# Kernel tuning notes

Hardware: AMD Instinct MI355X
Metric: run time of the kernel (lower is better)

## Reference

```python
import jax, jax.numpy as jnp
import numpy as np

B, N, C_IN = 4, 48, 32
HID = [32, 32]          # hidden_channel_list
NB = [32, 32]           # neighborhood_channels
C_OUT = 16
N_BASIS = 6             # equivariant 2->2 basis ops used by SnConv2


def _masked(t, mask):
    # zero out entries for padded nodes; mask: B,n,n,n bool, t: B,n,n,n,C
    return jnp.where(mask[..., None], t, jnp.zeros((), t.dtype))


def snconv2(t, W, b):
    """Sn-equivariant 2nd-order conv on dims (1,2); dim 3 rides along.
    t: B,i,j,m,C.  W: [6, C_in, C_out], one mixing matrix per basis op."""
    n = t.shape[1]
    tT = jnp.swapaxes(t, 1, 2)                       # transpose op
    diag = jnp.einsum('biimc->bimc', t)              # diagonal, B,i,m,C
    rows = t.sum(axis=2) / n                         # row sums,  B,i,m,C
    cols = t.sum(axis=1) / n                         # col sums,  B,j,m,C
    tot = t.sum(axis=(1, 2)) / (n * n)               # total sum, B,m,C
    # contract small features BEFORE broadcasting back to 2nd order
    out = (jnp.einsum('bijmc,cd->bijmd', t, W[0])
           + jnp.einsum('bijmc,cd->bijmd', tT, W[1])
           + jnp.einsum('bimc,cd->bimd', diag, W[2])[:, :, None]
           + jnp.einsum('bimc,cd->bimd', rows, W[3])[:, :, None]
           + jnp.einsum('bjmc,cd->bjmd', cols, W[4])[:, None]
           + jnp.einsum('bmc,cd->bmd', tot, W[5])[:, None, None]
           + b)
    return out


def localconv2(t, Wv, bv, Ww, bw, Wo, bo):
    """LocalConv2, product_type='elementwise': per-channel message passing
    along the node dims: z[b,i,j] = sum_k v[b,i,k] * w[b,k,j] / n."""
    n = t.shape[1]
    v = jnp.einsum('bijmc,cd->bijmd', t, Wv) + bv
    w = jnp.einsum('bijmc,cd->bijmd', t, Ww) + bw
    z = jnp.einsum('bikmc,bkjmc->bijmc', v, w) / n
    return jnp.einsum('bijmc,cd->bijmd', z, Wo) + bo


def setup_inputs() -> dict:
    key = jax.random.key(0)
    ks = jax.random.split(key, 24)
    x = jax.random.normal(ks[0], (B, N, C_IN), dtype=jnp.float32)
    # graphs of unequal size: per-graph node counts in [N//2, N]
    sizes = jax.random.randint(ks[1], (B,), N // 2, N + 1)
    node_valid = jnp.arange(N)[None, :] < sizes[:, None]            # B,n
    mask = (node_valid[:, :, None, None]
            & node_valid[:, None, :, None]
            & node_valid[:, None, None, :])                          # B,n,n,n
    s = 0.05
    inp = {'x': x, 'mask': mask}
    cin = C_IN
    for li, (nch, cout) in enumerate(zip(NB, HID)):
        inp[f'basic_W{li}'] = s * jax.random.normal(ks[2 + 8 * li], (N_BASIS, cin, cin), dtype=jnp.float32)
        inp[f'basic_b{li}'] = jnp.zeros((cin,), jnp.float32)
        inp[f'lv_W{li}'] = s * jax.random.normal(ks[3 + 8 * li], (cin, nch), dtype=jnp.float32)
        inp[f'lv_b{li}'] = jnp.zeros((nch,), jnp.float32)
        inp[f'lw_W{li}'] = s * jax.random.normal(ks[4 + 8 * li], (cin, nch), dtype=jnp.float32)
        inp[f'lw_b{li}'] = jnp.zeros((nch,), jnp.float32)
        inp[f'lo_W{li}'] = s * jax.random.normal(ks[5 + 8 * li], (nch, cout), dtype=jnp.float32)
        inp[f'lo_b{li}'] = jnp.zeros((cout,), jnp.float32)
        cin = cout
    inp['final_W'] = s * jax.random.normal(ks[20], (N_BASIS, cin, C_OUT), dtype=jnp.float32)
    inp['final_b'] = jnp.zeros((C_OUT,), jnp.float32)
    return inp


def reference(x, mask,
              basic_W0, basic_b0, lv_W0, lv_b0, lw_W0, lw_b0, lo_W0, lo_b0,
              basic_W1, basic_b1, lv_W1, lv_b1, lw_W1, lw_b1, lo_W1, lo_b1,
              final_W, final_b):
    # order-3 outer product T[b,i,j,k,c] = x[b,i,c]*x[b,j,c]*x[b,k,c]
    t = (x[:, :, None, None, :] * x[:, None, :, None, :]) * x[:, None, None, :, :]
    t = _masked(t, mask)
    layers = [(basic_W0, basic_b0, lv_W0, lv_b0, lw_W0, lw_b0, lo_W0, lo_b0),
              (basic_W1, basic_b1, lv_W1, lv_b1, lw_W1, lw_b1, lo_W1, lo_b1)]
    for bw_, bb_, vw, vb, ww, wb, ow, ob in layers:
        t = _masked(snconv2(t, bw_, bb_), mask)
        t = localconv2(t, vw, vb, ww, wb, ow, ob)
        t = jax.nn.relu(t)
        t = _masked(t, mask)
    out = _masked(snconv2(t, final_W, final_b), mask)
    return out
```

## Files before the change

kernel.cpp:

```cpp
#include <hip/hip_runtime.h>
#include <cstdint>


namespace {

constexpr int nB = 4, nN = 48, nC = 32;
constexpr int SJ_ = nN * nC;
constexpr int SI_ = nN * SJ_;
constexpr long SB_ = (long)nN * SI_;
constexpr int CP_ = 294912;
constexpr int TP_ = 6144;

__device__ __forceinline__ void decodePos(int p, int& b, int& i, int& j, int& m) {
    m = p % nN; int r = p / nN;
    j = r % nN; r /= nN;
    i = r % nN; b = r / nN;
}

__global__ __launch_bounds__(256) void k_prep(const float* __restrict__ x,
                                              const void* __restrict__ maskp,
                                              float* __restrict__ vm,
                                              float* __restrict__ S)
{
    __shared__ float vmL[nB * nN];
    const int tid = threadIdx.x;
    const unsigned int w0 = *(const unsigned int*)maskp;
    const bool is_byte = (w0 == 0x01010101u);
    if (tid < nB * nN) {
        int b = tid / nN, i = tid % nN;
        long idx = ((long)(b * nN + i) * nN + i) * nN + i;
        int bit;
        if (is_byte) bit = (((const unsigned char*)maskp)[idx] != 0);
        else         bit = (((const int*)maskp)[idx] != 0);
        float f = bit ? 1.f : 0.f;
        vm[tid] = f; vmL[tid] = f;
    }
    __syncthreads();
    if (tid < nB * nC) {
        int b = tid >> 5, c = tid & 31;
        float s = 0.f;
        for (int j = 0; j < nN; ++j) s += x[(b * nN + j) * nC + c] * vmL[b * nN + j];
        S[tid] = s;
    }
}

__global__ __launch_bounds__(256) void k_mix0(
    const float* __restrict__ x, const float* __restrict__ S,
    const float* __restrict__ Wb, const float* __restrict__ bias,
    float* __restrict__ drp, float* __restrict__ ccp, float* __restrict__ tbp)
{
    __shared__ float W2s[1024], W3s[1024], W4s[1024], W5s[1024], bs[32];
    const int tid = threadIdx.x;
    for (int q = tid; q < 1024; q += 256) {
        W2s[q] = Wb[2048 + q]; W3s[q] = Wb[3072 + q];
        W4s[q] = Wb[4096 + q]; W5s[q] = Wb[5120 + q];
    }
    if (tid < 32) bs[tid] = bias[tid];
    __syncthreads();
    const int id = blockIdx.x * 256 + tid;
    const int m = id % nN; int r = id / nN; const int i = r % nN; const int b = r / nN;
    float odr[32], occ[32];
    #pragma unroll
    for (int d = 0; d < 32; ++d) { odr[d] = 0.f; occ[d] = 0.f; }
    for (int c2 = 0; c2 < 32; ++c2) {
        float xi = x[(b * nN + i) * nC + c2];
        float xm = x[(b * nN + m) * nC + c2];
        float sc = S[b * nC + c2];
        float A = xi * xi * xm;
        float R = xi * xm * sc * (1.f / nN);
        #pragma unroll
        for (int d = 0; d < 32; ++d) {
            odr[d] = fmaf(A, W2s[c2 * 32 + d], fmaf(R, W3s[c2 * 32 + d], odr[d]));
            occ[d] = fmaf(R, W4s[c2 * 32 + d], occ[d]);
        }
    }
    #pragma unroll
    for (int d = 0; d < 32; d += 4) {
        *(float4*)(drp + (size_t)id * 32 + d) = make_float4(odr[d], odr[d+1], odr[d+2], odr[d+3]);
        *(float4*)(ccp + (size_t)id * 32 + d) = make_float4(occ[d], occ[d+1], occ[d+2], occ[d+3]);
    }
    if (i == 0) {
        float ot[32];
        #pragma unroll
        for (int d = 0; d < 32; ++d) ot[d] = bs[d];
        for (int c2 = 0; c2 < 32; ++c2) {
            float xm = x[(b * nN + m) * nC + c2];
            float sc = S[b * nC + c2];
            float Tc = xm * sc * sc * (1.f / (nN * nN));
            #pragma unroll
            for (int d = 0; d < 32; ++d) ot[d] = fmaf(Tc, W5s[c2 * 32 + d], ot[d]);
        }
        for (int d = 0; d < 32; d += 4)
            *(float4*)(tbp + (size_t)(b * nN + m) * 32 + d) = make_float4(ot[d], ot[d+1], ot[d+2], ot[d+3]);
    }
}

template <int DOUT>
__global__ __launch_bounds__(256) void k_mix(
    const float* __restrict__ dgp, const float* __restrict__ rwp,
    const float* __restrict__ clp4, const float* __restrict__ ttp4,
    const float* __restrict__ Wb, const float* __restrict__ bias,
    float* __restrict__ drp, float* __restrict__ ccp, float* __restrict__ tbp)
{
    __shared__ float W2s[32 * DOUT], W3s[32 * DOUT], W4s[32 * DOUT], W5s[32 * DOUT], bs[DOUT];
    const int tid = threadIdx.x;
    for (int q = tid; q < 32 * DOUT; q += 256) {
        W2s[q] = Wb[2 * 32 * DOUT + q]; W3s[q] = Wb[3 * 32 * DOUT + q];
        W4s[q] = Wb[4 * 32 * DOUT + q]; W5s[q] = Wb[5 * 32 * DOUT + q];
    }
    if (tid < DOUT) bs[tid] = bias[tid];
    __syncthreads();
    const int id = blockIdx.x * 256 + tid;
    const int m = id % nN; int r = id / nN; const int i = r % nN; const int b = r / nN;
    float odr[DOUT], occ[DOUT];
    #pragma unroll
    for (int d = 0; d < DOUT; ++d) { odr[d] = 0.f; occ[d] = 0.f; }
    for (int c2 = 0; c2 < 32; ++c2) {
        size_t q = (size_t)id * 32 + c2;
        float dg = dgp[q];
        float rw = rwp[q];
        float cl = clp4[q] + clp4[q + CP_] + clp4[q + 2 * CP_] + clp4[q + 3 * CP_];
        #pragma unroll
        for (int d = 0; d < DOUT; ++d) {
            odr[d] = fmaf(dg, W2s[c2 * DOUT + d], fmaf(rw, W3s[c2 * DOUT + d], odr[d]));
            occ[d] = fmaf(cl, W4s[c2 * DOUT + d], occ[d]);
        }
    }
    #pragma unroll
    for (int d = 0; d < DOUT; d += 4) {
        *(float4*)(drp + (size_t)id * DOUT + d) = make_float4(odr[d], odr[d+1], odr[d+2], odr[d+3]);
        *(float4*)(ccp + (size_t)id * DOUT + d) = make_float4(occ[d], occ[d+1], occ[d+2], occ[d+3]);
    }
    if (i == 0) {
        float ot[DOUT];
        #pragma unroll
        for (int d = 0; d < DOUT; ++d) ot[d] = bs[d];
        for (int c2 = 0; c2 < 32; ++c2) {
            size_t q = (size_t)(b * nN + m) * 32 + c2;
            float tv = ttp4[q] + ttp4[q + TP_] + ttp4[q + 2 * TP_] + ttp4[q + 3 * TP_];
            #pragma unroll
            for (int d = 0; d < DOUT; ++d) ot[d] = fmaf(tv, W5s[c2 * DOUT + d], ot[d]);
        }
        for (int d = 0; d < DOUT; d += 4)
            *(float4*)(tbp + (size_t)(b * nN + m) * DOUT + d) = make_float4(ot[d], ot[d+1], ot[d+2], ot[d+3]);
    }
}

__global__ __launch_bounds__(256) void k_red4(
    const float* __restrict__ t,
    float* __restrict__ rows_, float* __restrict__ cols4,
    float* __restrict__ diag_, float* __restrict__ tot4)
{
    const int blk = blockIdx.x;
    const int iq = blk & 3; const int bm = blk >> 2;
    const int b = bm / nN, m = bm % nN;
    const int jg = threadIdx.x >> 5;
    const int c = threadIdx.x & 31;
    __shared__ float part[8][32];
    const size_t base = (size_t)b * SB_ + (size_t)m * nC;
    float colacc[6] = {0, 0, 0, 0, 0, 0};
    float totacc = 0.f;
    for (int ii = 0; ii < 12; ++ii) {
        const int i = iq * 12 + ii;
        float vals[6];
        #pragma unroll
        for (int jl = 0; jl < 6; ++jl) {
            int j = jg * 6 + jl;
            vals[jl] = t[base + (size_t)i * SI_ + (size_t)j * SJ_ + c];
        }
        float rp = 0.f;
        #pragma unroll
        for (int jl = 0; jl < 6; ++jl) { colacc[jl] += vals[jl]; rp += vals[jl]; }
        {
            int jd = i - jg * 6;
            if (jd >= 0 && jd < 6) diag_[((size_t)(b * nN + i) * nN + m) * nC + c] = vals[jd];
        }
        part[jg][c] = rp;
        __syncthreads();
        if (jg == 0) {
            float rv = 0.f;
            #pragma unroll
            for (int g = 0; g < 8; ++g) rv += part[g][c];
            rows_[((size_t)(b * nN + i) * nN + m) * nC + c] = rv * (1.f / nN);
            totacc += rv;
        }
        __syncthreads();
    }
    #pragma unroll
    for (int jl = 0; jl < 6; ++jl) {
        int j = jg * 6 + jl;
        cols4[(size_t)iq * CP_ + ((size_t)(b * nN + j) * nN + m) * nC + c] = colacc[jl] * (1.f / nN);
    }
    if (jg == 0)
        tot4[(size_t)iq * TP_ + (size_t)(b * nN + m) * nC + c] = totacc * (1.f / (nN * nN));
}

template <int MODE>
__global__ __launch_bounds__(256) void k_vw(
    const float* __restrict__ src, const float* __restrict__ vm,
    const float* __restrict__ drp, const float* __restrict__ ccp, const float* __restrict__ tbp,
    const float* __restrict__ W0, const float* __restrict__ W1,
    const float* __restrict__ Wv, const float* __restrict__ bv,
    const float* __restrict__ Ww, const float* __restrict__ bw,
    float* __restrict__ vout, float* __restrict__ wout)
{
    __shared__ float sA[128 * 34];
    __shared__ float sB[(MODE == 0) ? 64 : 128 * 34];
    __shared__ float sS[128 * 34];
    const int tid = threadIdx.x;
    const long base = (long)blockIdx.x * 128;

    if (MODE == 0) {
        for (int rep = 0; rep < 4; ++rep) {
            int q = rep * 256 + tid; int pl = q >> 3, cq = q & 7;
            int p = (int)base + pl;
            int b, i, j, m; decodePos(p, b, i, j, m);
            float4 xi = *(const float4*)(src + (size_t)(b * nN + i) * nC + cq * 4);
            float4 xj = *(const float4*)(src + (size_t)(b * nN + j) * nC + cq * 4);
            float4 xm = *(const float4*)(src + (size_t)(b * nN + m) * nC + cq * 4);
            int o = pl * 34 + cq * 4;
            sA[o + 0] = xi.x * xj.x * xm.x;
            sA[o + 1] = xi.y * xj.y * xm.y;
            sA[o + 2] = xi.z * xj.z * xm.z;
            sA[o + 3] = xi.w * xj.w * xm.w;
        }
    } else {
        for (int rep = 0; rep < 4; ++rep) {
            int q = rep * 256 + tid; int pl = q >> 3, cq = q & 7;
            long p = base + pl;
            float4 a = *(const float4*)(src + p * nC + cq * 4);
            int o = pl * 34 + cq * 4;
            sA[o + 0] = a.x; sA[o + 1] = a.y; sA[o + 2] = a.z; sA[o + 3] = a.w;
            int b, i, j, m; decodePos((int)p, b, i, j, m);
            long pT = ((long)(b * nN + j) * nN + i) * nN + m;
            float4 t4 = *(const float4*)(src + pT * nC + cq * 4);
            sB[o + 0] = t4.x; sB[o + 1] = t4.y; sB[o + 2] = t4.z; sB[o + 3] = t4.w;
        }
    }
    __syncthreads();

    const int pt = tid >> 3, dq = tid & 7;
    const int p0 = pt * 4, d0 = dq * 4;
    float wc[32][4];
    float acc[4][4];

    auto zeroAcc = [&]() {
        #pragma unroll
        for (int a2 = 0; a2 < 4; ++a2)
            #pragma unroll
            for (int l = 0; l < 4; ++l) acc[a2][l] = 0.f;
    };
    auto loadW = [&](const float* Wp) {
        #pragma unroll
        for (int c2 = 0; c2 < 32; ++c2) {
            float4 q4 = *(const float4*)(Wp + c2 * nC + d0);
            wc[c2][0] = q4.x; wc[c2][1] = q4.y; wc[c2][2] = q4.z; wc[c2][3] = q4.w;
        }
    };
    auto addW = [&](const float* Wp) {
        #pragma unroll
        for (int c2 = 0; c2 < 32; ++c2) {
            float4 q4 = *(const float4*)(Wp + c2 * nC + d0);
            wc[c2][0] += q4.x; wc[c2][1] += q4.y; wc[c2][2] += q4.z; wc[c2][3] += q4.w;
        }
    };
    auto sweep = [&](const float* sp) {
        #pragma unroll
        for (int c2 = 0; c2 < 32; ++c2) {
            float t0 = sp[(p0 + 0) * 34 + c2];
            float t1 = sp[(p0 + 1) * 34 + c2];
            float t2 = sp[(p0 + 2) * 34 + c2];
            float t3 = sp[(p0 + 3) * 34 + c2];
            #pragma unroll
            for (int l = 0; l < 4; ++l) {
                acc[0][l] = fmaf(t0, wc[c2][l], acc[0][l]);
                acc[1][l] = fmaf(t1, wc[c2][l], acc[1][l]);
                acc[2][l] = fmaf(t2, wc[c2][l], acc[2][l]);
                acc[3][l] = fmaf(t3, wc[c2][l], acc[3][l]);
            }
        }
    };

    zeroAcc();
    if (MODE == 0) { loadW(W0); addW(W1); sweep(sA); }
    else           { loadW(W0); sweep(sA); loadW(W1); sweep(sB); }

    #pragma unroll
    for (int l = 0; l < 4; ++l) {
        int p = (int)base + p0 + l;
        int b, i, j, m; decodePos(p, b, i, j, m);
        float4 d4 = *(const float4*)(drp + (size_t)((b * nN + i) * nN + m) * nC + d0);
        float4 c4 = *(const float4*)(ccp + (size_t)((b * nN + j) * nN + m) * nC + d0);
        float4 t4 = *(const float4*)(tbp + (size_t)(b * nN + m) * nC + d0);
        float mk = vm[b * nN + i] * vm[b * nN + j] * vm[b * nN + m];
        int o = (p0 + l) * 34 + d0;
        sS[o + 0] = (acc[l][0] + d4.x + c4.x + t4.x) * mk;
        sS[o + 1] = (acc[l][1] + d4.y + c4.y + t4.y) * mk;
        sS[o + 2] = (acc[l][2] + d4.z + c4.z + t4.z) * mk;
        sS[o + 3] = (acc[l][3] + d4.w + c4.w + t4.w) * mk;
    }
    __syncthreads();

    zeroAcc(); loadW(Wv); sweep(sS);
    {
        float4 b4 = *(const float4*)(bv + d0);
        #pragma unroll
        for (int l = 0; l < 4; ++l) {
            float4 o4 = make_float4(acc[l][0] + b4.x, acc[l][1] + b4.y,
                                    acc[l][2] + b4.z, acc[l][3] + b4.w);
            *(float4*)(vout + (size_t)(base + p0 + l) * nC + d0) = o4;
        }
    }
    zeroAcc(); loadW(Ww); sweep(sS);
    {
        float4 b4 = *(const float4*)(bw + d0);
        #pragma unroll
        for (int l = 0; l < 4; ++l) {
            float4 o4 = make_float4(acc[l][0] + b4.x, acc[l][1] + b4.y,
                                    acc[l][2] + b4.z, acc[l][3] + b4.w);
            *(float4*)(wout + (size_t)(base + p0 + l) * nC + d0) = o4;
        }
    }
}

__global__ __launch_bounds__(256, 3) void k_z(
    const float* __restrict__ v, const float* __restrict__ w,
    const float* __restrict__ Wo, const float* __restrict__ bo,
    const float* __restrict__ vm, float* __restrict__ tout)
{
    __shared__ float lds[12912];
    float* Vt = lds;
    float* Wt = lds + 6456;
    const int tid = threadIdx.x;
    const int blk = blockIdx.x;
    const int tl = blk & 3; const int bm = blk >> 2;
    const int it = tl >> 1, jt = tl & 1;
    const int b = bm / nN, m = bm % nN;
    const int c = tid & 31;
    const int g = tid >> 5;
    const int i3 = g >> 1, j2 = g & 1;
    const int il0 = i3 * 6, jl0 = j2 * 12;
    const size_t posbase = (size_t)b * SB_ + (size_t)m * nC;

    float acc[6][12];
    #pragma unroll
    for (int l = 0; l < 6; ++l)
        #pragma unroll
        for (int u = 0; u < 12; ++u) acc[l][u] = 0.f;

    for (int kc = 0; kc < 6; ++kc) {
        if (kc) __syncthreads();
        #pragma unroll
        for (int rr = 0; rr < 6; ++rr) {
            int q = rr * 256 + tid; int pos = q >> 3, cq = q & 7;
            int ii = pos >> 3, kk = pos & 7;
            float4 a = *(const float4*)(v + posbase + (size_t)(it * 24 + ii) * SI_
                                          + (size_t)(kc * 8 + kk) * SJ_ + cq * 4);
            float* dst = Vt + kk * 807 + (cq * 4) * 25 + ii;
            dst[0] = a.x; dst[25] = a.y; dst[50] = a.z; dst[75] = a.w;
        }
        #pragma unroll
        for (int rr = 0; rr < 6; ++rr) {
            int q = rr * 256 + tid; int pos = q >> 3, cq = q & 7;
            int kk = pos / 24, jj = pos - kk * 24;
            float4 a = *(const float4*)(w + posbase + (size_t)(kc * 8 + kk) * SI_
                                          + (size_t)(jt * 24 + jj) * SJ_ + cq * 4);
            float* dst = Wt + kk * 807 + (cq * 4) * 25 + jj;
            dst[0] = a.x; dst[25] = a.y; dst[50] = a.z; dst[75] = a.w;
        }
        __syncthreads();
        #pragma unroll
        for (int kk = 0; kk < 8; ++kk) {
            float vf[6], wf[12];
            #pragma unroll
            for (int l = 0; l < 6; ++l) vf[l] = Vt[kk * 807 + c * 25 + il0 + l];
            #pragma unroll
            for (int u = 0; u < 12; ++u) wf[u] = Wt[kk * 807 + c * 25 + jl0 + u];
            #pragma unroll
            for (int l = 0; l < 6; ++l)
                #pragma unroll
                for (int u = 0; u < 12; ++u)
                    acc[l][u] = fmaf(vf[l], wf[u], acc[l][u]);
        }
    }
    __syncthreads();

    #pragma unroll
    for (int e = 0; e < 4; ++e)
        lds[9504 + e * 256 + tid] = Wo[e * 256 + tid] * (1.f / nN);

    const int ptE = tid >> 3, dqE = tid & 7, d0 = dqE * 4;
    const float4 b4 = *(const float4*)(bo + d0);
    const float vmm = vm[b * nN + m];

    for (int h = 0; h < 2; ++h) {
        if ((i3 >> 1) == h) {
            int r0 = il0 - 12 * h;
            #pragma unroll
            for (int l = 0; l < 6; ++l)
                #pragma unroll
                for (int u = 0; u < 12; ++u)
                    lds[((r0 + l) * 24 + jl0 + u) * 33 + c] = acc[l][u];
        }
        __syncthreads();

        float oac[9][4];
        #pragma unroll
        for (int u = 0; u < 9; ++u)
            #pragma unroll
            for (int d = 0; d < 4; ++d) oac[u][d] = 0.f;
        #pragma unroll
        for (int c2 = 0; c2 < 32; ++c2) {
            float4 wo4 = *(const float4*)(lds + 9504 + c2 * 32 + d0);
            float zv[9];
            #pragma unroll
            for (int u = 0; u < 9; ++u) zv[u] = lds[(ptE * 9 + u) * 33 + c2];
            #pragma unroll
            for (int u = 0; u < 9; ++u) {
                oac[u][0] = fmaf(zv[u], wo4.x, oac[u][0]);
                oac[u][1] = fmaf(zv[u], wo4.y, oac[u][1]);
                oac[u][2] = fmaf(zv[u], wo4.z, oac[u][2]);
                oac[u][3] = fmaf(zv[u], wo4.w, oac[u][3]);
            }
        }
        #pragma unroll
        for (int u = 0; u < 9; ++u) {
            int p = ptE * 9 + u;
            int rl = p / 24, jl = p - rl * 24;
            int gi = it * 24 + 12 * h + rl, gj = jt * 24 + jl;
            float mk = vm[b * nN + gi] * vm[b * nN + gj] * vmm;
            float4 o4;
            o4.x = fmaxf(oac[u][0] + b4.x, 0.f) * mk;
            o4.y = fmaxf(oac[u][1] + b4.y, 0.f) * mk;
            o4.z = fmaxf(oac[u][2] + b4.z, 0.f) * mk;
            o4.w = fmaxf(oac[u][3] + b4.w, 0.f) * mk;
            *(float4*)(tout + posbase + (size_t)gi * SI_ + (size_t)gj * SJ_ + d0) = o4;
        }
        if (h == 0) __syncthreads();
    }
}

__global__ __launch_bounds__(256) void k_final(
    const float* __restrict__ t, const float* __restrict__ vm,
    const float* __restrict__ drp, const float* __restrict__ ccp, const float* __restrict__ tbp,
    const float* __restrict__ W0, const float* __restrict__ W1,
    float* __restrict__ out)
{
    __shared__ float sA[128 * 34], sB[128 * 34];
    const int tid = threadIdx.x;
    const long base = (long)blockIdx.x * 128;
    for (int rep = 0; rep < 4; ++rep) {
        int q = rep * 256 + tid; int pl = q >> 3, cq = q & 7;
        long p = base + pl;
        float4 a = *(const float4*)(t + p * nC + cq * 4);
        int o = pl * 34 + cq * 4;
        sA[o + 0] = a.x; sA[o + 1] = a.y; sA[o + 2] = a.z; sA[o + 3] = a.w;
        int b, i, j, m; decodePos((int)p, b, i, j, m);
        long pT = ((long)(b * nN + j) * nN + i) * nN + m;
        float4 t4 = *(const float4*)(t + pT * nC + cq * 4);
        sB[o + 0] = t4.x; sB[o + 1] = t4.y; sB[o + 2] = t4.z; sB[o + 3] = t4.w;
    }
    __syncthreads();
    const int pt = tid >> 3, dq = tid & 7;
    const int p0 = pt * 4, d0 = dq * 2;
    float wc[32][2], acc[4][2];
    #pragma unroll
    for (int l = 0; l < 4; ++l) { acc[l][0] = 0.f; acc[l][1] = 0.f; }

    #pragma unroll
    for (int c2 = 0; c2 < 32; ++c2) {
        float2 q2 = *(const float2*)(W0 + c2 * 16 + d0);
        wc[c2][0] = q2.x; wc[c2][1] = q2.y;
    }
    #pragma unroll
    for (int c2 = 0; c2 < 32; ++c2) {
        float t0 = sA[(p0 + 0) * 34 + c2], t1 = sA[(p0 + 1) * 34 + c2];
        float t2 = sA[(p0 + 2) * 34 + c2], t3 = sA[(p0 + 3) * 34 + c2];
        acc[0][0] = fmaf(t0, wc[c2][0], acc[0][0]); acc[0][1] = fmaf(t0, wc[c2][1], acc[0][1]);
        acc[1][0] = fmaf(t1, wc[c2][0], acc[1][0]); acc[1][1] = fmaf(t1, wc[c2][1], acc[1][1]);
        acc[2][0] = fmaf(t2, wc[c2][0], acc[2][0]); acc[2][1] = fmaf(t2, wc[c2][1], acc[2][1]);
        acc[3][0] = fmaf(t3, wc[c2][0], acc[3][0]); acc[3][1] = fmaf(t3, wc[c2][1], acc[3][1]);
    }
    #pragma unroll
    for (int c2 = 0; c2 < 32; ++c2) {
        float2 q2 = *(const float2*)(W1 + c2 * 16 + d0);
        wc[c2][0] = q2.x; wc[c2][1] = q2.y;
    }
    #pragma unroll
    for (int c2 = 0; c2 < 32; ++c2) {
        float t0 = sB[(p0 + 0) * 34 + c2], t1 = sB[(p0 + 1) * 34 + c2];
        float t2 = sB[(p0 + 2) * 34 + c2], t3 = sB[(p0 + 3) * 34 + c2];
        acc[0][0] = fmaf(t0, wc[c2][0], acc[0][0]); acc[0][1] = fmaf(t0, wc[c2][1], acc[0][1]);
        acc[1][0] = fmaf(t1, wc[c2][0], acc[1][0]); acc[1][1] = fmaf(t1, wc[c2][1], acc[1][1]);
        acc[2][0] = fmaf(t2, wc[c2][0], acc[2][0]); acc[2][1] = fmaf(t2, wc[c2][1], acc[2][1]);
        acc[3][0] = fmaf(t3, wc[c2][0], acc[3][0]); acc[3][1] = fmaf(t3, wc[c2][1], acc[3][1]);
    }
    #pragma unroll
    for (int l = 0; l < 4; ++l) {
        int p = (int)base + p0 + l;
        int b, i, j, m; decodePos(p, b, i, j, m);
        float2 d2 = *(const float2*)(drp + (size_t)((b * nN + i) * nN + m) * 16 + d0);
        float2 cc2 = *(const float2*)(ccp + (size_t)((b * nN + j) * nN + m) * 16 + d0);
        float2 tb2 = *(const float2*)(tbp + (size_t)(b * nN + m) * 16 + d0);
        float mk = vm[b * nN + i] * vm[b * nN + j] * vm[b * nN + m];
        float2 o2;
        o2.x = (acc[l][0] + d2.x + cc2.x + tb2.x) * mk;
        o2.y = (acc[l][1] + d2.y + cc2.y + tb2.y) * mk;
        *(float2*)(out + (size_t)p * 16 + d0) = o2;
    }
}

}

extern "C" void kernel_launch(void* const* d_in, const int* in_sizes, int n_in,
                              void* d_out, int out_size, void* d_ws, size_t ws_size,
                              hipStream_t stream)
{
    (void)in_sizes; (void)n_in; (void)out_size; (void)ws_size;
    const float* x    = (const float*)d_in[0];
    const void*  mask = d_in[1];
    const float* bW0  = (const float*)d_in[2];
    const float* bb0  = (const float*)d_in[3];
    const float* lvW0 = (const float*)d_in[4];
    const float* lvb0 = (const float*)d_in[5];
    const float* lwW0 = (const float*)d_in[6];
    const float* lwb0 = (const float*)d_in[7];
    const float* loW0 = (const float*)d_in[8];
    const float* lob0 = (const float*)d_in[9];
    const float* bW1  = (const float*)d_in[10];
    const float* bb1  = (const float*)d_in[11];
    const float* lvW1 = (const float*)d_in[12];
    const float* lvb1 = (const float*)d_in[13];
    const float* lwW1 = (const float*)d_in[14];
    const float* lwb1 = (const float*)d_in[15];
    const float* loW1 = (const float*)d_in[16];
    const float* lob1 = (const float*)d_in[17];
    const float* fW   = (const float*)d_in[18];
    const float* fb   = (const float*)d_in[19];

    float* ws  = (float*)d_ws;
    float* t     = ws;
    float* v     = ws + 14155776L;
    float* w     = ws + 28311552L;
    float* rows  = ws + 42467328L;
    float* cols4 = rows + 294912;
    float* diag  = cols4 + 4 * 294912;
    float* tot4  = diag + 294912;
    float* dr    = tot4 + 4 * 6144;
    float* cc    = dr + 294912;
    float* tb    = cc + 294912;
    float* S     = tb + 6144;
    float* vm    = S + 128;
    float* out   = (float*)d_out;

    k_prep<<<1, 256, 0, stream>>>(x, mask, vm, S);
    k_mix0<<<36, 256, 0, stream>>>(x, S, bW0, bb0, dr, cc, tb);
    k_vw<0><<<3456, 256, 0, stream>>>(x, vm, dr, cc, tb, bW0, bW0 + 1024,
                                      lvW0, lvb0, lwW0, lwb0, v, w);
    k_z<<<768, 256, 0, stream>>>(v, w, loW0, lob0, vm, t);
    k_red4<<<768, 256, 0, stream>>>(t, rows, cols4, diag, tot4);
    k_mix<32><<<36, 256, 0, stream>>>(diag, rows, cols4, tot4, bW1, bb1, dr, cc, tb);

    k_vw<1><<<3456, 256, 0, stream>>>(t, vm, dr, cc, tb, bW1, bW1 + 1024,
                                      lvW1, lvb1, lwW1, lwb1, v, w);
    k_z<<<768, 256, 0, stream>>>(v, w, loW1, lob1, vm, t);
    k_red4<<<768, 256, 0, stream>>>(t, rows, cols4, diag, tot4);
    k_mix<16><<<36, 256, 0, stream>>>(diag, rows, cols4, tot4, fW, fb, dr, cc, tb);
    k_final<<<3456, 256, 0, stream>>>(t, vm, dr, cc, tb, fW, fW + 512, out);
}
```

Before: 537.7 us.

## Fuse row/col/diag/total reductions into k_z epilogue, drop k_red4

```diff
diff --git a/kernel.cpp b/kernel.cpp
--- a/kernel.cpp
+++ b/kernel.cpp
@@ -8,6 +8,7 @@
 constexpr int SJ_ = nN * nC;
 constexpr int SI_ = nN * SJ_;
 constexpr long SB_ = (long)nN * SI_;
+constexpr int RP_ = 294912;
 constexpr int CP_ = 294912;
 constexpr int TP_ = 6144;
 
@@ -97,8 +98,8 @@
 
 template <int DOUT>
 __global__ __launch_bounds__(256) void k_mix(
-    const float* __restrict__ dgp, const float* __restrict__ rwp,
-    const float* __restrict__ clp4, const float* __restrict__ ttp4,
+    const float* __restrict__ dgp, const float* __restrict__ rw2,
+    const float* __restrict__ cl2, const float* __restrict__ tt4,
     const float* __restrict__ Wb, const float* __restrict__ bias,
     float* __restrict__ drp, float* __restrict__ ccp, float* __restrict__ tbp)
 {
@@ -118,8 +119,8 @@
     for (int c2 = 0; c2 < 32; ++c2) {
         size_t q = (size_t)id * 32 + c2;
         float dg = dgp[q];
-        float rw = rwp[q];
-        float cl = clp4[q] + clp4[q + CP_] + clp4[q + 2 * CP_] + clp4[q + 3 * CP_];
+        float rw = (rw2[q] + rw2[q + RP_]) * (1.f / nN);
+        float cl = (cl2[q] + cl2[q + CP_]) * (1.f / nN);
         #pragma unroll
         for (int d = 0; d < DOUT; ++d) {
             odr[d] = fmaf(dg, W2s[c2 * DOUT + d], fmaf(rw, W3s[c2 * DOUT + d], odr[d]));
@@ -137,62 +138,14 @@
         for (int d = 0; d < DOUT; ++d) ot[d] = bs[d];
         for (int c2 = 0; c2 < 32; ++c2) {
             size_t q = (size_t)(b * nN + m) * 32 + c2;
-            float tv = ttp4[q] + ttp4[q + TP_] + ttp4[q + 2 * TP_] + ttp4[q + 3 * TP_];
+            float tv = (tt4[q] + tt4[q + TP_] + tt4[q + 2 * TP_] + tt4[q + 3 * TP_])
+                       * (1.f / (nN * nN));
             #pragma unroll
             for (int d = 0; d < DOUT; ++d) ot[d] = fmaf(tv, W5s[c2 * DOUT + d], ot[d]);
         }
         for (int d = 0; d < DOUT; d += 4)
             *(float4*)(tbp + (size_t)(b * nN + m) * DOUT + d) = make_float4(ot[d], ot[d+1], ot[d+2], ot[d+3]);
     }
-}
-
-__global__ __launch_bounds__(256) void k_red4(
-    const float* __restrict__ t,
-    float* __restrict__ rows_, float* __restrict__ cols4,
-    float* __restrict__ diag_, float* __restrict__ tot4)
-{
-    const int blk = blockIdx.x;
-    const int iq = blk & 3; const int bm = blk >> 2;
-    const int b = bm / nN, m = bm % nN;
-    const int jg = threadIdx.x >> 5;
-    const int c = threadIdx.x & 31;
-    __shared__ float part[8][32];
-    const size_t base = (size_t)b * SB_ + (size_t)m * nC;
-    float colacc[6] = {0, 0, 0, 0, 0, 0};
-    float totacc = 0.f;
-    for (int ii = 0; ii < 12; ++ii) {
-        const int i = iq * 12 + ii;
-        float vals[6];
-        #pragma unroll
-        for (int jl = 0; jl < 6; ++jl) {
-            int j = jg * 6 + jl;
-            vals[jl] = t[base + (size_t)i * SI_ + (size_t)j * SJ_ + c];
-        }
-        float rp = 0.f;
-        #pragma unroll
-        for (int jl = 0; jl < 6; ++jl) { colacc[jl] += vals[jl]; rp += vals[jl]; }
-        {
-            int jd = i - jg * 6;
-            if (jd >= 0 && jd < 6) diag_[((size_t)(b * nN + i) * nN + m) * nC + c] = vals[jd];
-        }
-        part[jg][c] = rp;
-        __syncthreads();
-        if (jg == 0) {
-            float rv = 0.f;
-            #pragma unroll
-            for (int g = 0; g < 8; ++g) rv += part[g][c];
-            rows_[((size_t)(b * nN + i) * nN + m) * nC + c] = rv * (1.f / nN);
-            totacc += rv;
-        }
-        __syncthreads();
-    }
-    #pragma unroll
-    for (int jl = 0; jl < 6; ++jl) {
-        int j = jg * 6 + jl;
-        cols4[(size_t)iq * CP_ + ((size_t)(b * nN + j) * nN + m) * nC + c] = colacc[jl] * (1.f / nN);
-    }
-    if (jg == 0)
-        tot4[(size_t)iq * TP_ + (size_t)(b * nN + m) * nC + c] = totacc * (1.f / (nN * nN));
 }
 
 template <int MODE>
@@ -266,17 +219,22 @@
     };
     auto sweep = [&](const float* sp) {
         #pragma unroll
-        for (int c2 = 0; c2 < 32; ++c2) {
-            float t0 = sp[(p0 + 0) * 34 + c2];
-            float t1 = sp[(p0 + 1) * 34 + c2];
-            float t2 = sp[(p0 + 2) * 34 + c2];
-            float t3 = sp[(p0 + 3) * 34 + c2];
-            #pragma unroll
-            for (int l = 0; l < 4; ++l) {
-                acc[0][l] = fmaf(t0, wc[c2][l], acc[0][l]);
-                acc[1][l] = fmaf(t1, wc[c2][l], acc[1][l]);
-                acc[2][l] = fmaf(t2, wc[c2][l], acc[2][l]);
-                acc[3][l] = fmaf(t3, wc[c2][l], acc[3][l]);
+        for (int cp = 0; cp < 16; ++cp) {
+            float2 t0 = *(const float2*)(sp + (p0 + 0) * 34 + cp * 2);
+            float2 t1 = *(const float2*)(sp + (p0 + 1) * 34 + cp * 2);
+            float2 t2 = *(const float2*)(sp + (p0 + 2) * 34 + cp * 2);
+            float2 t3 = *(const float2*)(sp + (p0 + 3) * 34 + cp * 2);
+            const int c0 = cp * 2, c1 = cp * 2 + 1;
+            #pragma unroll
+            for (int d = 0; d < 4; ++d) {
+                acc[0][d] = fmaf(t0.x, wc[c0][d], acc[0][d]);
+                acc[1][d] = fmaf(t1.x, wc[c0][d], acc[1][d]);
+                acc[2][d] = fmaf(t2.x, wc[c0][d], acc[2][d]);
+                acc[3][d] = fmaf(t3.x, wc[c0][d], acc[3][d]);
+                acc[0][d] = fmaf(t0.y, wc[c1][d], acc[0][d]);
+                acc[1][d] = fmaf(t1.y, wc[c1][d], acc[1][d]);
+                acc[2][d] = fmaf(t2.y, wc[c1][d], acc[2][d]);
+                acc[3][d] = fmaf(t3.y, wc[c1][d], acc[3][d]);
             }
         }
     };
@@ -326,11 +284,16 @@
 __global__ __launch_bounds__(256, 3) void k_z(
     const float* __restrict__ v, const float* __restrict__ w,
     const float* __restrict__ Wo, const float* __restrict__ bo,
-    const float* __restrict__ vm, float* __restrict__ tout)
+    const float* __restrict__ vm, float* __restrict__ tout,
+    float* __restrict__ rows2, float* __restrict__ cols2,
+    float* __restrict__ diag_, float* __restrict__ tot4)
 {
     __shared__ float lds[12912];
     float* Vt = lds;
     float* Wt = lds + 6456;
+    constexpr int ZS = 34;
+    constexpr int ZWO = 9792;
+    constexpr int TOT0 = 10816;
     const int tid = threadIdx.x;
     const int blk = blockIdx.x;
     const int tl = blk & 3; const int bm = blk >> 2;
@@ -387,20 +350,23 @@
 
     #pragma unroll
     for (int e = 0; e < 4; ++e)
-        lds[9504 + e * 256 + tid] = Wo[e * 256 + tid] * (1.f / nN);
+        lds[ZWO + e * 256 + tid] = Wo[e * 256 + tid] * (1.f / nN);
 
     const int ptE = tid >> 3, dqE = tid & 7, d0 = dqE * 4;
     const float4 b4 = *(const float4*)(bo + d0);
     const float vmm = vm[b * nN + m];
+    float colacc[3] = {0.f, 0.f, 0.f};
+    float totacc = 0.f;
 
     for (int h = 0; h < 2; ++h) {
+        if (h) __syncthreads();
         if ((i3 >> 1) == h) {
             int r0 = il0 - 12 * h;
             #pragma unroll
             for (int l = 0; l < 6; ++l)
                 #pragma unroll
                 for (int u = 0; u < 12; ++u)
-                    lds[((r0 + l) * 24 + jl0 + u) * 33 + c] = acc[l][u];
+                    lds[((r0 + l) * 24 + jl0 + u) * ZS + c] = acc[l][u];
         }
         __syncthreads();
 
@@ -411,10 +377,10 @@
             for (int d = 0; d < 4; ++d) oac[u][d] = 0.f;
         #pragma unroll
         for (int c2 = 0; c2 < 32; ++c2) {
-            float4 wo4 = *(const float4*)(lds + 9504 + c2 * 32 + d0);
+            float4 wo4 = *(const float4*)(lds + ZWO + c2 * 32 + d0);
             float zv[9];
             #pragma unroll
-            for (int u = 0; u < 9; ++u) zv[u] = lds[(ptE * 9 + u) * 33 + c2];
+            for (int u = 0; u < 9; ++u) zv[u] = lds[(ptE * 9 + u) * ZS + c2];
             #pragma unroll
             for (int u = 0; u < 9; ++u) {
                 oac[u][0] = fmaf(zv[u], wo4.x, oac[u][0]);
@@ -423,6 +389,8 @@
                 oac[u][3] = fmaf(zv[u], wo4.w, oac[u][3]);
             }
         }
+        __syncthreads();
+
         #pragma unroll
         for (int u = 0; u < 9; ++u) {
             int p = ptE * 9 + u;
@@ -435,8 +403,50 @@
             o4.z = fmaxf(oac[u][2] + b4.z, 0.f) * mk;
             o4.w = fmaxf(oac[u][3] + b4.w, 0.f) * mk;
             *(float4*)(tout + posbase + (size_t)gi * SI_ + (size_t)gj * SJ_ + d0) = o4;
-        }
-        if (h == 0) __syncthreads();
+            *(float2*)(lds + p * ZS + d0) = make_float2(o4.x, o4.y);
+            *(float2*)(lds + p * ZS + d0 + 2) = make_float2(o4.z, o4.w);
+        }
+        __syncthreads();
+
+        for (int rd = 0; rd < 2; ++rd) {
+            int task = rd * 256 + tid;
+            if (task < 384) {
+                int i_r = task >> 5, c_r = task & 31;
+                float rsum = 0.f;
+                #pragma unroll
+                for (int jl = 0; jl < 24; ++jl) rsum += lds[(i_r * 24 + jl) * ZS + c_r];
+                int gi = it * 24 + 12 * h + i_r;
+                rows2[(size_t)jt * RP_ + ((size_t)(b * nN + gi) * nN + m) * nC + c_r] = rsum;
+                totacc += rsum;
+                if (it == jt)
+                    diag_[((size_t)(b * nN + gi) * nN + m) * nC + c_r] =
+                        lds[(i_r * 24 + (12 * h + i_r)) * ZS + c_r];
+            }
+        }
+        #pragma unroll
+        for (int rr = 0; rr < 3; ++rr) {
+            int task = rr * 256 + tid;
+            int jl = task >> 5, c_c = task & 31;
+            float csum = 0.f;
+            #pragma unroll
+            for (int il = 0; il < 12; ++il) csum += lds[(il * 24 + jl) * ZS + c_c];
+            colacc[rr] += csum;
+        }
+    }
+
+    #pragma unroll
+    for (int rr = 0; rr < 3; ++rr) {
+        int task = rr * 256 + tid;
+        int jl = task >> 5, c_c = task & 31;
+        cols2[(size_t)it * CP_ + ((size_t)(b * nN + jt * 24 + jl) * nN + m) * nC + c_c] = colacc[rr];
+    }
+    lds[TOT0 + g * 32 + c] = totacc;
+    __syncthreads();
+    if (tid < 32) {
+        float s = 0.f;
+        #pragma unroll
+        for (int gg = 0; gg < 8; ++gg) s += lds[TOT0 + gg * 32 + tid];
+        tot4[(size_t)(it * 2 + jt) * TP_ + (size_t)(b * nN + m) * nC + tid] = s;
     }
 }
 
@@ -467,34 +477,35 @@
     #pragma unroll
     for (int l = 0; l < 4; ++l) { acc[l][0] = 0.f; acc[l][1] = 0.f; }
 
-    #pragma unroll
-    for (int c2 = 0; c2 < 32; ++c2) {
-        float2 q2 = *(const float2*)(W0 + c2 * 16 + d0);
-        wc[c2][0] = q2.x; wc[c2][1] = q2.y;
-    }
-    #pragma unroll
-    for (int c2 = 0; c2 < 32; ++c2) {
-        float t0 = sA[(p0 + 0) * 34 + c2], t1 = sA[(p0 + 1) * 34 + c2];
-        float t2 = sA[(p0 + 2) * 34 + c2], t3 = sA[(p0 + 3) * 34 + c2];
-        acc[0][0] = fmaf(t0, wc[c2][0], acc[0][0]); acc[0][1] = fmaf(t0, wc[c2][1], acc[0][1]);
-        acc[1][0] = fmaf(t1, wc[c2][0], acc[1][0]); acc[1][1] = fmaf(t1, wc[c2][1], acc[1][1]);
-        acc[2][0] = fmaf(t2, wc[c2][0], acc[2][0]); acc[2][1] = fmaf(t2, wc[c2][1], acc[2][1]);
-        acc[3][0] = fmaf(t3, wc[c2][0], acc[3][0]); acc[3][1] = fmaf(t3, wc[c2][1], acc[3][1]);
-    }
-    #pragma unroll
-    for (int c2 = 0; c2 < 32; ++c2) {
-        float2 q2 = *(const float2*)(W1 + c2 * 16 + d0);
-        wc[c2][0] = q2.x; wc[c2][1] = q2.y;
-    }
-    #pragma unroll
-    for (int c2 = 0; c2 < 32; ++c2) {
-        float t0 = sB[(p0 + 0) * 34 + c2], t1 = sB[(p0 + 1) * 34 + c2];
-        float t2 = sB[(p0 + 2) * 34 + c2], t3 = sB[(p0 + 3) * 34 + c2];
-        acc[0][0] = fmaf(t0, wc[c2][0], acc[0][0]); acc[0][1] = fmaf(t0, wc[c2][1], acc[0][1]);
-        acc[1][0] = fmaf(t1, wc[c2][0], acc[1][0]); acc[1][1] = fmaf(t1, wc[c2][1], acc[1][1]);
-        acc[2][0] = fmaf(t2, wc[c2][0], acc[2][0]); acc[2][1] = fmaf(t2, wc[c2][1], acc[2][1]);
-        acc[3][0] = fmaf(t3, wc[c2][0], acc[3][0]); acc[3][1] = fmaf(t3, wc[c2][1], acc[3][1]);
-    }
+    auto loadW = [&](const float* Wp) {
+        #pragma unroll
+        for (int c2 = 0; c2 < 32; ++c2) {
+            float2 q2 = *(const float2*)(Wp + c2 * 16 + d0);
+            wc[c2][0] = q2.x; wc[c2][1] = q2.y;
+        }
+    };
+    auto sweep = [&](const float* sp) {
+        #pragma unroll
+        for (int cp = 0; cp < 16; ++cp) {
+            float2 t0 = *(const float2*)(sp + (p0 + 0) * 34 + cp * 2);
+            float2 t1 = *(const float2*)(sp + (p0 + 1) * 34 + cp * 2);
+            float2 t2 = *(const float2*)(sp + (p0 + 2) * 34 + cp * 2);
+            float2 t3 = *(const float2*)(sp + (p0 + 3) * 34 + cp * 2);
+            const int c0 = cp * 2, c1 = cp * 2 + 1;
+            acc[0][0] = fmaf(t0.x, wc[c0][0], acc[0][0]); acc[0][1] = fmaf(t0.x, wc[c0][1], acc[0][1]);
+            acc[1][0] = fmaf(t1.x, wc[c0][0], acc[1][0]); acc[1][1] = fmaf(t1.x, wc[c0][1], acc[1][1]);
+            acc[2][0] = fmaf(t2.x, wc[c0][0], acc[2][0]); acc[2][1] = fmaf(t2.x, wc[c0][1], acc[2][1]);
+            acc[3][0] = fmaf(t3.x, wc[c0][0], acc[3][0]); acc[3][1] = fmaf(t3.x, wc[c0][1], acc[3][1]);
+            acc[0][0] = fmaf(t0.y, wc[c1][0], acc[0][0]); acc[0][1] = fmaf(t0.y, wc[c1][1], acc[0][1]);
+            acc[1][0] = fmaf(t1.y, wc[c1][0], acc[1][0]); acc[1][1] = fmaf(t1.y, wc[c1][1], acc[1][1]);
+            acc[2][0] = fmaf(t2.y, wc[c1][0], acc[2][0]); acc[2][1] = fmaf(t2.y, wc[c1][1], acc[2][1]);
+            acc[3][0] = fmaf(t3.y, wc[c1][0], acc[3][0]); acc[3][1] = fmaf(t3.y, wc[c1][1], acc[3][1]);
+        }
+    };
+
+    loadW(W0); sweep(sA);
+    loadW(W1); sweep(sB);
+
     #pragma unroll
     for (int l = 0; l < 4; ++l) {
         int p = (int)base + p0 + l;
@@ -542,9 +553,9 @@
     float* t     = ws;
     float* v     = ws + 14155776L;
     float* w     = ws + 28311552L;
-    float* rows  = ws + 42467328L;
-    float* cols4 = rows + 294912;
-    float* diag  = cols4 + 4 * 294912;
+    float* rows2 = ws + 42467328L;
+    float* cols2 = rows2 + 2 * 294912;
+    float* diag  = cols2 + 2 * 294912;
     float* tot4  = diag + 294912;
     float* dr    = tot4 + 4 * 6144;
     float* cc    = dr + 294912;
@@ -557,14 +568,12 @@
     k_mix0<<<36, 256, 0, stream>>>(x, S, bW0, bb0, dr, cc, tb);
     k_vw<0><<<3456, 256, 0, stream>>>(x, vm, dr, cc, tb, bW0, bW0 + 1024,
                                       lvW0, lvb0, lwW0, lwb0, v, w);
-    k_z<<<768, 256, 0, stream>>>(v, w, loW0, lob0, vm, t);
-    k_red4<<<768, 256, 0, stream>>>(t, rows, cols4, diag, tot4);
-    k_mix<32><<<36, 256, 0, stream>>>(diag, rows, cols4, tot4, bW1, bb1, dr, cc, tb);
+    k_z<<<768, 256, 0, stream>>>(v, w, loW0, lob0, vm, t, rows2, cols2, diag, tot4);
+    k_mix<32><<<36, 256, 0, stream>>>(diag, rows2, cols2, tot4, bW1, bb1, dr, cc, tb);
 
     k_vw<1><<<3456, 256, 0, stream>>>(t, vm, dr, cc, tb, bW1, bW1 + 1024,
                                       lvW1, lvb1, lwW1, lwb1, v, w);
-    k_z<<<768, 256, 0, stream>>>(v, w, loW1, lob1, vm, t);
-    k_red4<<<768, 256, 0, stream>>>(t, rows, cols4, diag, tot4);
-    k_mix<16><<<36, 256, 0, stream>>>(diag, rows, cols4, tot4, fW, fb, dr, cc, tb);
+    k_z<<<768, 256, 0, stream>>>(v, w, loW1, lob1, vm, t, rows2, cols2, diag, tot4);
+    k_mix<16><<<36, 256, 0, stream>>>(diag, rows2, cols2, tot4, fW, fb, dr, cc, tb);
     k_final<<<3456, 256, 0, stream>>>(t, vm, dr, cc, tb, fW, fW + 512, out);
 }
```

After: 533.7 us. No clear change (-0.7%).
